# Kernel optimization log

Measured on AMD Instinct MI355X. Metric: run time of the kernel, lower is better.

## Reference

```python
import jax, jax.numpy as jnp
import numpy as np

EP = 1e-4
MAX_ITER = 100
L = [512, 512]          # context lengths
C = 256                 # padded feature dim == total_dim
HEADS = 2


def nonsat_activation(x, ep=EP, max_iter=MAX_ITER):
    # Fixed-point iteration y <- (2y^3/3 + x)/(y^2+1), y0 = x.
    # Matches torch version: iterate on detached values, final update uses live x.
    xd = jax.lax.stop_gradient(x)
    f = lambda y: (2.0 * y ** 3 / 3.0 + xd) / (y ** 2 + 1.0)

    def cond(s):
        y, y_new, i = s
        return jnp.logical_and(jnp.mean(jnp.abs(y_new - y)) > ep, i <= max_iter)

    def body(s):
        y, y_new, i = s
        return (y_new, f(y_new), i + 1)

    y_prev, _, _ = jax.lax.while_loop(cond, body, (xd, f(xd), 0))
    y_prev = jax.lax.stop_gradient(y_prev)
    # final (returned) update, differentiable w.r.t. x only
    return (2.0 * y_prev ** 3 / 3.0 + x) / (y_prev ** 2 + 1.0)


def setup_inputs() -> dict:
    key = jax.random.key(0)
    k1, k2, k3 = jax.random.split(key, 3)
    x1 = jax.random.normal(k1, (32, 512, 256), dtype=jnp.float32)
    x2 = jax.random.normal(k2, (32, 512, 192), dtype=jnp.float32)
    # xavier_normal_ for U: std = sqrt(2/(fan_in+fan_out)) = sqrt(2/512) = 1/16
    U = jax.random.normal(k3, (HEADS, C, C), dtype=jnp.float32) * (1.0 / 16.0)
    return {"x1": x1, "x2": x2, "U": U}


def reference(x1, x2, U):
    # pad contexts to common feature dim C (zeros on the right)
    contexts = [x1, jnp.pad(x2, ((0, 0), (0, 0), (0, C - x2.shape[-1])))]
    q = sum(L)
    scaling = C ** (-0.5)
    M = jnp.concatenate(contexts, axis=1)  # (B, q, C)

    # mask uses sizes = L[1:] with blocks starting at offset 0 (faithful quirk)
    mask_mul = jnp.ones((q, q), dtype=jnp.float32).at[:L[1], :L[1]].set(0.0)

    h_reps = []
    mask_add = None
    for h in range(HEADS):
        # K[b,i,j] = sum_{c,d} M[b,i,c] U[h,c,d] M[b,j,d]
        K = jnp.einsum('bic,cd,bjd->bij', M, U[h], M) * scaling
        K = nonsat_activation(K)
        if mask_add is None:  # cached after head 0, reused for later heads
            mask_add = jnp.zeros((q, q), dtype=jnp.float32).at[:L[1], :L[1]].set(jnp.min(K))
        K_hat = K * mask_mul + mask_add
        cols = jnp.max(K_hat, axis=1)   # (B, q) max over rows per column
        rows = jnp.max(K_hat, axis=2)   # (B, q) max over cols per row
        alpha = rows + cols             # (B, q)
        reps = []
        offset = 0
        for i, Ci in enumerate(contexts):
            a = alpha[:, offset:offset + L[i]]          # (B, l_i)
            offset += L[i]
            wt = jax.nn.softmax(a, axis=1)              # (B, l_i)
            r = jnp.einsum('bl,blc->bc', wt, Ci)        # (B, C)
            reps.append(r)
        h_reps.append(jnp.stack(reps, axis=1))          # (B, N, C)
    return jnp.stack(h_reps, axis=0)                    # (heads, B, N, C)
```

## Files before the change

kernel.cpp:

```cpp
#include <hip/hip_runtime.h>
#include <math.h>

typedef _Float16 h16;
typedef h16  h16x8 __attribute__((ext_vector_type(8)));
typedef h16  h16x4 __attribute__((ext_vector_type(4)));
typedef float f32x4 __attribute__((ext_vector_type(4)));

#define MH_OFF   ((size_t)0)
#define ML_OFF   (MH_OFF + 16777216)
#define UHT_OFF  (ML_OFF + 16777216)
#define ULT_OFF  (UHT_OFF + 262144)
#define RMA_OFF  (ULT_OFF + 262144)
#define RMH_OFF  (RMA_OFF + 262144)
#define PCM_OFF  (RMH_OFF + 262144)
#define M0_OFF   (PCM_OFF + 4194304)

__device__ __forceinline__ float nonsat(float x) {
    float y = x;
#pragma unroll
    for (int i = 0; i < 24; ++i) {
        float y2 = y * y;
        y = fmaf(0.66666667f * y, y2, x) / (y2 + 1.0f);
    }
    return y;
}

__device__ __forceinline__ int fkey(float f) {
    const int i = __float_as_int(f);
    return (i >= 0) ? i : (i ^ 0x7fffffff);
}
__device__ __forceinline__ float funkey(int k) {
    return __int_as_float((k >= 0) ? k : (k ^ 0x7fffffff));
}

__global__ void k_prep(const float* __restrict__ x1, const float* __restrict__ x2,
                       const float* __restrict__ U, h16* __restrict__ MH,
                       h16* __restrict__ ML, h16* __restrict__ UHt,
                       h16* __restrict__ ULt, int* __restrict__ m0key) {
    const int gid = blockIdx.x * 256 + threadIdx.x;
    if (blockIdx.x < 8192) {
        const int g  = gid;
        const int d4 = (g & 63) * 4;
        const int j  = (g >> 6) & 1023;
        const int b  = g >> 16;
        float v[4];
        if (j < 512) {
            const float* p = x1 + ((size_t)(b * 512 + j) * 256 + d4);
#pragma unroll
            for (int k = 0; k < 4; ++k) v[k] = p[k];
        } else {
            const float* p = x2 + (size_t)(b * 512 + (j - 512)) * 192;
#pragma unroll
            for (int k = 0; k < 4; ++k) {
                const int c = d4 + k;
                v[k] = (c < 192) ? p[c] : 0.0f;
            }
        }
        h16x4 hh, ll;
#pragma unroll
        for (int k = 0; k < 4; ++k) {
            const h16 hi = (h16)v[k];
            hh[k] = hi;
            ll[k] = (h16)(v[k] - (float)hi);
        }
        const size_t o = (size_t)g * 4;
        *(h16x4*)&MH[o] = hh;
        *(h16x4*)&ML[o] = ll;
    } else {
        const int g = gid - 8192 * 256;
        if (g < 32768) {
            const int c4 = (g & 63) * 4;
            const int d  = (g >> 6) & 255;
            const int h  = g >> 14;
            h16x4 hh, ll;
#pragma unroll
            for (int k = 0; k < 4; ++k) {
                const float v = U[((size_t)h * 256 + c4 + k) * 256 + d] * 4.0f;
                const h16 hi = (h16)v;
                hh[k] = hi;
                ll[k] = (h16)(v - (float)hi);
            }
            const size_t o = ((size_t)h * 256 + d) * 256 + c4;
            *(h16x4*)&UHt[o] = hh;
            *(h16x4*)&ULt[o] = ll;
        } else if (g == 32768) {
            *m0key = 0x7fffffff;
        }
    }
}

__global__ __launch_bounds__(256, 2)
void k_main(const h16* __restrict__ MH, const h16* __restrict__ ML,
            const h16* __restrict__ UHt, const h16* __restrict__ ULt,
            float* __restrict__ rmax_all, float* __restrict__ rmax_hi,
            float* __restrict__ pcm, int* __restrict__ m0key) {
    __shared__ __align__(16) h16 sP[2][64 * 256];
    __shared__ float red[512 + 4];

    const int n    = blockIdx.x;
    const int x    = n & 7;
    const int s    = n >> 3;
    const int b    = x + 8 * (s >> 5);
    const int h    = (s >> 4) & 1;
    const int rblk = s & 15;
    const int hb   = h * 32 + b;
    const int r0   = rblk * 64;
    const int t    = threadIdx.x;
    const int w    = t >> 6;
    const int l    = t & 63;
    const int q    = l >> 4;
    const int ln   = l & 15;

    {
        f32x4 acc[4][4];
        const f32x4 z4 = {0.f, 0.f, 0.f, 0.f};
#pragma unroll
        for (int i = 0; i < 4; ++i)
#pragma unroll
            for (int j = 0; j < 4; ++j) acc[i][j] = z4;

        for (int kc = 0; kc < 8; ++kc) {
            const int c0 = kc * 32;
            h16x8 aH[4], aL[4], bH[4], bL[4];
#pragma unroll
            for (int ti = 0; ti < 4; ++ti) {
                const size_t off =
                    (size_t)(b * 1024 + r0 + ti * 16 + ln) * 256 + c0 + q * 8;
                aH[ti] = *(const h16x8*)&MH[off];
                aL[ti] = *(const h16x8*)&ML[off];
            }
#pragma unroll
            for (int tj = 0; tj < 4; ++tj) {
                const size_t off =
                    (size_t)(h * 256 + w * 64 + tj * 16 + ln) * 256 + c0 + q * 8;
                bH[tj] = *(const h16x8*)&UHt[off];
                bL[tj] = *(const h16x8*)&ULt[off];
            }
#pragma unroll
            for (int ti = 0; ti < 4; ++ti)
#pragma unroll
                for (int tj = 0; tj < 4; ++tj)
                    acc[ti][tj] = __builtin_amdgcn_mfma_f32_16x16x32_f16(
                        aH[ti], bH[tj], acc[ti][tj], 0, 0, 0);
#pragma unroll
            for (int ti = 0; ti < 4; ++ti)
#pragma unroll
                for (int tj = 0; tj < 4; ++tj)
                    acc[ti][tj] = __builtin_amdgcn_mfma_f32_16x16x32_f16(
                        aL[ti], bH[tj], acc[ti][tj], 0, 0, 0);
#pragma unroll
            for (int ti = 0; ti < 4; ++ti)
#pragma unroll
                for (int tj = 0; tj < 4; ++tj)
                    acc[ti][tj] = __builtin_amdgcn_mfma_f32_16x16x32_f16(
                        aH[ti], bL[tj], acc[ti][tj], 0, 0, 0);
        }
#pragma unroll
        for (int ti = 0; ti < 4; ++ti)
#pragma unroll
            for (int tj = 0; tj < 4; ++tj)
#pragma unroll
                for (int reg = 0; reg < 4; ++reg) {
                    const int r = ti * 16 + q * 4 + reg;
                    const int d = w * 64 + tj * 16 + ln;
                    const float v = acc[ti][tj][reg];
                    const h16 hi = (h16)v;
                    const h16 lo = (h16)(v - (float)hi);
                    const int off = r * 256 + (((d >> 3) ^ (r & 7)) << 3) + (d & 7);
                    sP[0][off] = hi;
                    sP[1][off] = lo;
                }
    }
    __syncthreads();

    float gmin = INFINITY;

    for (int jt = 0; jt < 2; ++jt) {
        const int jbase = jt * 512 + w * 128;
        f32x4 acc[4][8];
        const f32x4 z4 = {0.f, 0.f, 0.f, 0.f};
#pragma unroll
        for (int i = 0; i < 4; ++i)
#pragma unroll
            for (int j = 0; j < 8; ++j) acc[i][j] = z4;

        for (int kc = 0; kc < 8; ++kc) {
            const int d0 = kc * 32;
            h16x8 aH[4], aL[4], bb[8];
#pragma unroll
            for (int ti = 0; ti < 4; ++ti) {
                const int r = ti * 16 + ln;
                const int g = (kc * 4 + q) ^ (r & 7);
                aH[ti] = *(const h16x8*)&sP[0][r * 256 + g * 8];
                aL[ti] = *(const h16x8*)&sP[1][r * 256 + g * 8];
            }
#pragma unroll
            for (int tj = 0; tj < 8; ++tj)
                bb[tj] = *(const h16x8*)&MH[
                    (size_t)(b * 1024 + jbase + tj * 16 + ln) * 256 + d0 + q * 8];
#pragma unroll
            for (int tj = 0; tj < 8; ++tj)
#pragma unroll
                for (int ti = 0; ti < 4; ++ti)
                    acc[ti][tj] = __builtin_amdgcn_mfma_f32_16x16x32_f16(
                        aH[ti], bb[tj], acc[ti][tj], 0, 0, 0);
#pragma unroll
            for (int tj = 0; tj < 8; ++tj)
#pragma unroll
                for (int ti = 0; ti < 4; ++ti)
                    acc[ti][tj] = __builtin_amdgcn_mfma_f32_16x16x32_f16(
                        aL[ti], bb[tj], acc[ti][tj], 0, 0, 0);
#pragma unroll
            for (int tj = 0; tj < 8; ++tj)
                bb[tj] = *(const h16x8*)&ML[
                    (size_t)(b * 1024 + jbase + tj * 16 + ln) * 256 + d0 + q * 8];
#pragma unroll
            for (int tj = 0; tj < 8; ++tj)
#pragma unroll
                for (int ti = 0; ti < 4; ++ti)
                    acc[ti][tj] = __builtin_amdgcn_mfma_f32_16x16x32_f16(
                        aH[ti], bb[tj], acc[ti][tj], 0, 0, 0);
        }

#pragma unroll
        for (int ti = 0; ti < 4; ++ti)
#pragma unroll
            for (int reg = 0; reg < 4; ++reg) {
                float m = acc[ti][0][reg];
#pragma unroll
                for (int tj = 1; tj < 8; ++tj) m = fmaxf(m, acc[ti][tj][reg]);
                m = fmaxf(m, __shfl_xor(m, 1));
                m = fmaxf(m, __shfl_xor(m, 2));
                m = fmaxf(m, __shfl_xor(m, 4));
                m = fmaxf(m, __shfl_xor(m, 8));
                if (ln == 0)
                    red[(jt * 4 + w) * 64 + ti * 16 + q * 4 + reg] = m;
            }
#pragma unroll
        for (int tj = 0; tj < 8; ++tj) {
            float m = -INFINITY;
#pragma unroll
            for (int ti = 0; ti < 4; ++ti)
#pragma unroll
                for (int reg = 0; reg < 4; ++reg) m = fmaxf(m, acc[ti][tj][reg]);
            m = fmaxf(m, __shfl_xor(m, 16));
            m = fmaxf(m, __shfl_xor(m, 32));
            if (q == 0)
                pcm[(size_t)(hb * 16 + rblk) * 1024 + jbase + tj * 16 + ln] =
                    m * 0.015625f;
        }
#pragma unroll
        for (int ti = 0; ti < 4; ++ti)
#pragma unroll
            for (int tj = 0; tj < 8; ++tj)
#pragma unroll
                for (int reg = 0; reg < 4; ++reg)
                    gmin = fminf(gmin, acc[ti][tj][reg]);
    }

#pragma unroll
    for (int off = 1; off < 64; off <<= 1) gmin = fminf(gmin, __shfl_xor(gmin, off));
    if (l == 0) red[512 + w] = gmin;
    __syncthreads();

    if (t < 64) {
        float a = -INFINITY, hh = -INFINITY;
#pragma unroll
        for (int w2 = 0; w2 < 4; ++w2) {
            a  = fmaxf(a,  red[w2 * 64 + t]);
            const float v1 = red[(4 + w2) * 64 + t];
            a  = fmaxf(a, v1);
            hh = fmaxf(hh, v1);
        }
        rmax_all[(size_t)hb * 1024 + r0 + t] = a  * 0.015625f;
        rmax_hi [(size_t)hb * 1024 + r0 + t] = hh * 0.015625f;
    }
    if (t == 0 && hb < 32) {
        const float g4 = fminf(fminf(red[512], red[513]),
                               fminf(red[514], red[515])) * 0.015625f;
        atomicMin(m0key, fkey(g4));
    }
}

__global__ __launch_bounds__(256)
void k_fin(const float* __restrict__ rmax_all, const float* __restrict__ rmax_hi,
           const float* __restrict__ pcm, const int* __restrict__ m0key,
           const float* __restrict__ x1, const float* __restrict__ x2,
           float* __restrict__ out) {
    __shared__ float wv[512];
    __shared__ float sm[4], ss[4];
    const int blk = blockIdx.x;
    const int seg = blk & 1;
    const int hb  = blk >> 1;
    const int b   = hb & 31;
    const int t   = threadIdx.x;
    const float m0 = funkey(*m0key);

    float a2[2];
#pragma unroll
    for (int half = 0; half < 2; ++half) {
        const int i = seg * 512 + half * 256 + t;
        float rraw;
        if (seg == 0) rraw = fmaxf(m0, rmax_hi[(size_t)hb * 1024 + i]);
        else          rraw = rmax_all[(size_t)hb * 1024 + i];
        float call = -INFINITY, chi = -INFINITY;
#pragma unroll
        for (int rb = 0; rb < 16; ++rb) {
            const float v = pcm[(size_t)(hb * 16 + rb) * 1024 + i];
            call = fmaxf(call, v);
            if (rb >= 8) chi = fmaxf(chi, v);
        }
        const float craw = (seg == 0) ? fmaxf(m0, chi) : call;
        a2[half] = nonsat(rraw) + nonsat(craw);
    }
    const float a0 = a2[0], a1 = a2[1];

    float m = fmaxf(a0, a1);
#pragma unroll
    for (int off = 1; off < 64; off <<= 1) m = fmaxf(m, __shfl_xor(m, off));
    if ((t & 63) == 0) sm[t >> 6] = m;
    __syncthreads();
    const float amax = fmaxf(fmaxf(sm[0], sm[1]), fmaxf(sm[2], sm[3]));

    const float e0 = __expf(a0 - amax), e1 = __expf(a1 - amax);
    wv[t] = e0; wv[t + 256] = e1;
    float s = e0 + e1;
#pragma unroll
    for (int off = 1; off < 64; off <<= 1) s += __shfl_xor(s, off);
    if ((t & 63) == 0) ss[t >> 6] = s;
    __syncthreads();
    const float inv = 1.0f / (ss[0] + ss[1] + ss[2] + ss[3]);

    float acc = 0.0f;
    if (seg == 0) {
        const float* xp = x1 + (size_t)b * 512 * 256 + t;
#pragma unroll 4
        for (int l = 0; l < 512; ++l) acc = fmaf(wv[l], xp[(size_t)l * 256], acc);
        out[blk * 256 + t] = acc * inv;
    } else {
        if (t < 192) {
            const float* xp = x2 + (size_t)b * 512 * 192 + t;
#pragma unroll 4
            for (int l = 0; l < 512; ++l) acc = fmaf(wv[l], xp[(size_t)l * 192], acc);
            out[blk * 256 + t] = acc * inv;
        } else {
            out[blk * 256 + t] = 0.0f;
        }
    }
}

extern "C" void kernel_launch(void* const* d_in, const int* in_sizes, int n_in,
                              void* d_out, int out_size, void* d_ws, size_t ws_size,
                              hipStream_t stream) {
    const float* x1 = (const float*)d_in[0];
    const float* x2 = (const float*)d_in[1];
    const float* U  = (const float*)d_in[2];
    float* out = (float*)d_out;
    char* wsb  = (char*)d_ws;

    h16*   MHp  = (h16*)(wsb + MH_OFF);
    h16*   MLp  = (h16*)(wsb + ML_OFF);
    h16*   UHt  = (h16*)(wsb + UHT_OFF);
    h16*   ULt  = (h16*)(wsb + ULT_OFF);
    float* rma  = (float*)(wsb + RMA_OFF);
    float* rmh  = (float*)(wsb + RMH_OFF);
    float* pcm  = (float*)(wsb + PCM_OFF);
    int*   m0k  = (int*)(wsb + M0_OFF);

    hipLaunchKernelGGL(k_prep, dim3(8321), dim3(256), 0, stream, x1, x2, U,
                       MHp, MLp, UHt, ULt, m0k);
    hipLaunchKernelGGL(k_main, dim3(1024), dim3(256), 0, stream, MHp, MLp,
                       UHt, ULt, rma, rmh, pcm, m0k);
    hipLaunchKernelGGL(k_fin,  dim3(128),  dim3(256), 0, stream, rma, rmh,
                       pcm, m0k, x1, x2, out);
}
```

Before: 296.9 us.

## Halve k_main row tile to 32 rows, doubling blocks and occupancy

Shrinks each k_main block from 64 to 32 query rows and splits the column sweep into four 256-wide chunks, cutting accumulator registers and shared memory so four blocks can fit per CU instead of two. Row maxima are now carried in registers across chunks and reduced once at the end, rather than written to shared memory per chunk. The grid doubles to 2048 blocks and the per-column partial-max buffer doubles, so k_fin now reduces 32 partials per column. The cost is more re-reading of M and U per output and a smaller MFMA tile per wave, which lowers operand reuse.

```diff
diff --git a/kernel.cpp b/kernel.cpp
--- a/kernel.cpp
+++ b/kernel.cpp
@@ -13,7 +13,7 @@
 #define RMA_OFF  (ULT_OFF + 262144)
 #define RMH_OFF  (RMA_OFF + 262144)
 #define PCM_OFF  (RMH_OFF + 262144)
-#define M0_OFF   (PCM_OFF + 4194304)
+#define M0_OFF   (PCM_OFF + 8388608)
 
 __device__ __forceinline__ float nonsat(float x) {
     float y = x;
@@ -89,22 +89,22 @@
     }
 }
 
-__global__ __launch_bounds__(256, 2)
+__global__ __launch_bounds__(256, 4)
 void k_main(const h16* __restrict__ MH, const h16* __restrict__ ML,
             const h16* __restrict__ UHt, const h16* __restrict__ ULt,
             float* __restrict__ rmax_all, float* __restrict__ rmax_hi,
             float* __restrict__ pcm, int* __restrict__ m0key) {
-    __shared__ __align__(16) h16 sP[2][64 * 256];
-    __shared__ float red[512 + 4];
+    __shared__ __align__(16) h16 sP[2][32 * 256];
+    __shared__ float red[256 + 4];
 
     const int n    = blockIdx.x;
     const int x    = n & 7;
     const int s    = n >> 3;
-    const int b    = x + 8 * (s >> 5);
-    const int h    = (s >> 4) & 1;
-    const int rblk = s & 15;
+    const int b    = x + 8 * (s >> 6);
+    const int h    = (s >> 5) & 1;
+    const int rb   = s & 31;
     const int hb   = h * 32 + b;
-    const int r0   = rblk * 64;
+    const int r0   = rb * 32;
     const int t    = threadIdx.x;
     const int w    = t >> 6;
     const int l    = t & 63;
@@ -112,18 +112,18 @@
     const int ln   = l & 15;
 
     {
-        f32x4 acc[4][4];
+        f32x4 acc[2][4];
         const f32x4 z4 = {0.f, 0.f, 0.f, 0.f};
 #pragma unroll
-        for (int i = 0; i < 4; ++i)
+        for (int i = 0; i < 2; ++i)
 #pragma unroll
             for (int j = 0; j < 4; ++j) acc[i][j] = z4;
 
         for (int kc = 0; kc < 8; ++kc) {
             const int c0 = kc * 32;
-            h16x8 aH[4], aL[4], bH[4], bL[4];
-#pragma unroll
-            for (int ti = 0; ti < 4; ++ti) {
+            h16x8 aH[2], aL[2], bH[4], bL[4];
+#pragma unroll
+            for (int ti = 0; ti < 2; ++ti) {
                 const size_t off =
                     (size_t)(b * 1024 + r0 + ti * 16 + ln) * 256 + c0 + q * 8;
                 aH[ti] = *(const h16x8*)&MH[off];
@@ -137,26 +137,26 @@
                 bL[tj] = *(const h16x8*)&ULt[off];
             }
 #pragma unroll
-            for (int ti = 0; ti < 4; ++ti)
+            for (int ti = 0; ti < 2; ++ti)
 #pragma unroll
                 for (int tj = 0; tj < 4; ++tj)
                     acc[ti][tj] = __builtin_amdgcn_mfma_f32_16x16x32_f16(
                         aH[ti], bH[tj], acc[ti][tj], 0, 0, 0);
 #pragma unroll
-            for (int ti = 0; ti < 4; ++ti)
+            for (int ti = 0; ti < 2; ++ti)
 #pragma unroll
                 for (int tj = 0; tj < 4; ++tj)
                     acc[ti][tj] = __builtin_amdgcn_mfma_f32_16x16x32_f16(
                         aL[ti], bH[tj], acc[ti][tj], 0, 0, 0);
 #pragma unroll
-            for (int ti = 0; ti < 4; ++ti)
+            for (int ti = 0; ti < 2; ++ti)
 #pragma unroll
                 for (int tj = 0; tj < 4; ++tj)
                     acc[ti][tj] = __builtin_amdgcn_mfma_f32_16x16x32_f16(
                         aH[ti], bL[tj], acc[ti][tj], 0, 0, 0);
         }
 #pragma unroll
-        for (int ti = 0; ti < 4; ++ti)
+        for (int ti = 0; ti < 2; ++ti)
 #pragma unroll
             for (int tj = 0; tj < 4; ++tj)
 #pragma unroll
@@ -173,111 +173,128 @@
     }
     __syncthreads();
 
+    float rA[8], rH[8];
+#pragma unroll
+    for (int i = 0; i < 8; ++i) { rA[i] = -INFINITY; rH[i] = -INFINITY; }
     float gmin = INFINITY;
 
-    for (int jt = 0; jt < 2; ++jt) {
-        const int jbase = jt * 512 + w * 128;
-        f32x4 acc[4][8];
+    for (int jt = 0; jt < 4; ++jt) {
+        const int jbase = jt * 256 + w * 64;
+        f32x4 acc[2][4];
         const f32x4 z4 = {0.f, 0.f, 0.f, 0.f};
 #pragma unroll
-        for (int i = 0; i < 4; ++i)
-#pragma unroll
-            for (int j = 0; j < 8; ++j) acc[i][j] = z4;
+        for (int i = 0; i < 2; ++i)
+#pragma unroll
+            for (int j = 0; j < 4; ++j) acc[i][j] = z4;
 
         for (int kc = 0; kc < 8; ++kc) {
             const int d0 = kc * 32;
-            h16x8 aH[4], aL[4], bb[8];
-#pragma unroll
-            for (int ti = 0; ti < 4; ++ti) {
+            h16x8 aH[2], aL[2], bb[4];
+#pragma unroll
+            for (int ti = 0; ti < 2; ++ti) {
                 const int r = ti * 16 + ln;
                 const int g = (kc * 4 + q) ^ (r & 7);
                 aH[ti] = *(const h16x8*)&sP[0][r * 256 + g * 8];
                 aL[ti] = *(const h16x8*)&sP[1][r * 256 + g * 8];
             }
 #pragma unroll
-            for (int tj = 0; tj < 8; ++tj)
+            for (int tj = 0; tj < 4; ++tj)
                 bb[tj] = *(const h16x8*)&MH[
                     (size_t)(b * 1024 + jbase + tj * 16 + ln) * 256 + d0 + q * 8];
 #pragma unroll
-            for (int tj = 0; tj < 8; ++tj)
-#pragma unroll
-                for (int ti = 0; ti < 4; ++ti)
+            for (int tj = 0; tj < 4; ++tj)
+#pragma unroll
+                for (int ti = 0; ti < 2; ++ti)
                     acc[ti][tj] = __builtin_amdgcn_mfma_f32_16x16x32_f16(
                         aH[ti], bb[tj], acc[ti][tj], 0, 0, 0);
 #pragma unroll
-            for (int tj = 0; tj < 8; ++tj)
-#pragma unroll
-                for (int ti = 0; ti < 4; ++ti)
+            for (int tj = 0; tj < 4; ++tj)
+#pragma unroll
+                for (int ti = 0; ti < 2; ++ti)
                     acc[ti][tj] = __builtin_amdgcn_mfma_f32_16x16x32_f16(
                         aL[ti], bb[tj], acc[ti][tj], 0, 0, 0);
 #pragma unroll
-            for (int tj = 0; tj < 8; ++tj)
+            for (int tj = 0; tj < 4; ++tj)
                 bb[tj] = *(const h16x8*)&ML[
                     (size_t)(b * 1024 + jbase + tj * 16 + ln) * 256 + d0 + q * 8];
 #pragma unroll
-            for (int tj = 0; tj < 8; ++tj)
-#pragma unroll
-                for (int ti = 0; ti < 4; ++ti)
+            for (int tj = 0; tj < 4; ++tj)
+#pragma unroll
+                for (int ti = 0; ti < 2; ++ti)
                     acc[ti][tj] = __builtin_amdgcn_mfma_f32_16x16x32_f16(
                         aH[ti], bb[tj], acc[ti][tj], 0, 0, 0);
         }
 
-#pragma unroll
-        for (int ti = 0; ti < 4; ++ti)
+        const bool hij = (jt >= 2);
+#pragma unroll
+        for (int ti = 0; ti < 2; ++ti)
 #pragma unroll
             for (int reg = 0; reg < 4; ++reg) {
                 float m = acc[ti][0][reg];
-#pragma unroll
-                for (int tj = 1; tj < 8; ++tj) m = fmaxf(m, acc[ti][tj][reg]);
-                m = fmaxf(m, __shfl_xor(m, 1));
-                m = fmaxf(m, __shfl_xor(m, 2));
-                m = fmaxf(m, __shfl_xor(m, 4));
-                m = fmaxf(m, __shfl_xor(m, 8));
-                if (ln == 0)
-                    red[(jt * 4 + w) * 64 + ti * 16 + q * 4 + reg] = m;
-            }
-#pragma unroll
-        for (int tj = 0; tj < 8; ++tj) {
+                m = fmaxf(m, acc[ti][1][reg]);
+                m = fmaxf(m, acc[ti][2][reg]);
+                m = fmaxf(m, acc[ti][3][reg]);
+                const int idx = ti * 4 + reg;
+                rA[idx] = fmaxf(rA[idx], m);
+                if (hij) rH[idx] = fmaxf(rH[idx], m);
+            }
+#pragma unroll
+        for (int tj = 0; tj < 4; ++tj) {
             float m = -INFINITY;
 #pragma unroll
-            for (int ti = 0; ti < 4; ++ti)
+            for (int ti = 0; ti < 2; ++ti)
 #pragma unroll
                 for (int reg = 0; reg < 4; ++reg) m = fmaxf(m, acc[ti][tj][reg]);
             m = fmaxf(m, __shfl_xor(m, 16));
             m = fmaxf(m, __shfl_xor(m, 32));
             if (q == 0)
-                pcm[(size_t)(hb * 16 + rblk) * 1024 + jbase + tj * 16 + ln] =
+                pcm[(size_t)(hb * 32 + rb) * 1024 + jbase + tj * 16 + ln] =
                     m * 0.015625f;
         }
 #pragma unroll
-        for (int ti = 0; ti < 4; ++ti)
-#pragma unroll
-            for (int tj = 0; tj < 8; ++tj)
+        for (int ti = 0; ti < 2; ++ti)
+#pragma unroll
+            for (int tj = 0; tj < 4; ++tj)
 #pragma unroll
                 for (int reg = 0; reg < 4; ++reg)
                     gmin = fminf(gmin, acc[ti][tj][reg]);
     }
 
 #pragma unroll
+    for (int ti = 0; ti < 2; ++ti)
+#pragma unroll
+        for (int reg = 0; reg < 4; ++reg) {
+            const int idx = ti * 4 + reg;
+            float a = rA[idx], hh = rH[idx];
+#pragma unroll
+            for (int o2 = 1; o2 < 16; o2 <<= 1) {
+                a  = fmaxf(a,  __shfl_xor(a,  o2));
+                hh = fmaxf(hh, __shfl_xor(hh, o2));
+            }
+            if (ln == 0) {
+                const int row = ti * 16 + q * 4 + reg;
+                red[w * 32 + row]       = a;
+                red[128 + w * 32 + row] = hh;
+            }
+        }
+#pragma unroll
     for (int off = 1; off < 64; off <<= 1) gmin = fminf(gmin, __shfl_xor(gmin, off));
-    if (l == 0) red[512 + w] = gmin;
+    if (l == 0) red[256 + w] = gmin;
     __syncthreads();
 
-    if (t < 64) {
+    if (t < 32) {
         float a = -INFINITY, hh = -INFINITY;
 #pragma unroll
         for (int w2 = 0; w2 < 4; ++w2) {
-            a  = fmaxf(a,  red[w2 * 64 + t]);
-            const float v1 = red[(4 + w2) * 64 + t];
-            a  = fmaxf(a, v1);
-            hh = fmaxf(hh, v1);
+            a  = fmaxf(a,  red[w2 * 32 + t]);
+            hh = fmaxf(hh, red[128 + w2 * 32 + t]);
         }
         rmax_all[(size_t)hb * 1024 + r0 + t] = a  * 0.015625f;
         rmax_hi [(size_t)hb * 1024 + r0 + t] = hh * 0.015625f;
     }
     if (t == 0 && hb < 32) {
-        const float g4 = fminf(fminf(red[512], red[513]),
-                               fminf(red[514], red[515])) * 0.015625f;
+        const float g4 = fminf(fminf(red[256], red[257]),
+                               fminf(red[258], red[259])) * 0.015625f;
         atomicMin(m0key, fkey(g4));
     }
 }
@@ -305,10 +322,10 @@
         else          rraw = rmax_all[(size_t)hb * 1024 + i];
         float call = -INFINITY, chi = -INFINITY;
 #pragma unroll
-        for (int rb = 0; rb < 16; ++rb) {
-            const float v = pcm[(size_t)(hb * 16 + rb) * 1024 + i];
+        for (int rb = 0; rb < 32; ++rb) {
+            const float v = pcm[(size_t)(hb * 32 + rb) * 1024 + i];
             call = fmaxf(call, v);
-            if (rb >= 8) chi = fmaxf(chi, v);
+            if (rb >= 16) chi = fmaxf(chi, v);
         }
         const float craw = (seg == 0) ? fmaxf(m0, chi) : call;
         a2[half] = nonsat(rraw) + nonsat(craw);
@@ -369,7 +386,7 @@
 
     hipLaunchKernelGGL(k_prep, dim3(8321), dim3(256), 0, stream, x1, x2, U,
                        MHp, MLp, UHt, ULt, m0k);
-    hipLaunchKernelGGL(k_main, dim3(1024), dim3(256), 0, stream, MHp, MLp,
+    hipLaunchKernelGGL(k_main, dim3(2048), dim3(256), 0, stream, MHp, MLp,
                        UHt, ULt, rma, rmh, pcm, m0k);
     hipLaunchKernelGGL(k_fin,  dim3(128),  dim3(256), 0, stream, rma, rmh,
                        pcm, m0k, x1, x2, out);
```

Measured after the change: 536.9 us. 80.8% more time.

## Shrink second GEMM tile to 4x4 per wave and accumulate row maxima in registers

Applied to the files above, without the earlier changes.

The second-stage GEMM now uses four column passes of 64 columns per wave instead of two passes of 128, halving the accumulator array so register pressure drops and occupancy may rise. Row maxima are kept in per-thread registers across passes and reduced with shuffles once at the end, replacing per-pass LDS writes. Both hi and lo B fragments are loaded up front, the k-loops are partially unrolled, and x1 is read with a vectorized float4 load in the prep kernel. The trade-off is that each A fragment from LDS is reused across fewer columns, so LDS traffic and loop overhead per MFMA increase.

```diff
diff --git a/kernel.cpp b/kernel.cpp
--- a/kernel.cpp
+++ b/kernel.cpp
@@ -45,9 +45,8 @@
         const int b  = g >> 16;
         float v[4];
         if (j < 512) {
-            const float* p = x1 + ((size_t)(b * 512 + j) * 256 + d4);
-#pragma unroll
-            for (int k = 0; k < 4; ++k) v[k] = p[k];
+            const float4 p = *(const float4*)(x1 + ((size_t)(b * 512 + j) * 256 + d4));
+            v[0] = p.x; v[1] = p.y; v[2] = p.z; v[3] = p.w;
         } else {
             const float* p = x2 + (size_t)(b * 512 + (j - 512)) * 192;
 #pragma unroll
@@ -119,6 +118,7 @@
 #pragma unroll
             for (int j = 0; j < 4; ++j) acc[i][j] = z4;
 
+#pragma unroll 2
         for (int kc = 0; kc < 8; ++kc) {
             const int c0 = kc * 32;
             h16x8 aH[4], aL[4], bH[4], bL[4];
@@ -173,20 +173,31 @@
     }
     __syncthreads();
 
+    float rA[16], rH[16];
+#pragma unroll
+    for (int i = 0; i < 16; ++i) { rA[i] = -INFINITY; rH[i] = -INFINITY; }
     float gmin = INFINITY;
 
-    for (int jt = 0; jt < 2; ++jt) {
-        const int jbase = jt * 512 + w * 128;
-        f32x4 acc[4][8];
+    for (int jt = 0; jt < 4; ++jt) {
+        const int jbase = jt * 256 + w * 64;
+        f32x4 acc[4][4];
         const f32x4 z4 = {0.f, 0.f, 0.f, 0.f};
 #pragma unroll
         for (int i = 0; i < 4; ++i)
 #pragma unroll
-            for (int j = 0; j < 8; ++j) acc[i][j] = z4;
-
+            for (int j = 0; j < 4; ++j) acc[i][j] = z4;
+
+#pragma unroll 2
         for (int kc = 0; kc < 8; ++kc) {
             const int d0 = kc * 32;
-            h16x8 aH[4], aL[4], bb[8];
+            h16x8 bbH[4], bbL[4], aH[4], aL[4];
+#pragma unroll
+            for (int tj = 0; tj < 4; ++tj) {
+                const size_t off =
+                    (size_t)(b * 1024 + jbase + tj * 16 + ln) * 256 + d0 + q * 8;
+                bbH[tj] = *(const h16x8*)&MH[off];
+                bbL[tj] = *(const h16x8*)&ML[off];
+            }
 #pragma unroll
             for (int ti = 0; ti < 4; ++ti) {
                 const int r = ti * 16 + ln;
@@ -195,49 +206,40 @@
                 aL[ti] = *(const h16x8*)&sP[1][r * 256 + g * 8];
             }
 #pragma unroll
-            for (int tj = 0; tj < 8; ++tj)
-                bb[tj] = *(const h16x8*)&MH[
-                    (size_t)(b * 1024 + jbase + tj * 16 + ln) * 256 + d0 + q * 8];
-#pragma unroll
-            for (int tj = 0; tj < 8; ++tj)
+            for (int tj = 0; tj < 4; ++tj)
 #pragma unroll
                 for (int ti = 0; ti < 4; ++ti)
                     acc[ti][tj] = __builtin_amdgcn_mfma_f32_16x16x32_f16(
-                        aH[ti], bb[tj], acc[ti][tj], 0, 0, 0);
-#pragma unroll
-            for (int tj = 0; tj < 8; ++tj)
+                        aH[ti], bbH[tj], acc[ti][tj], 0, 0, 0);
+#pragma unroll
+            for (int tj = 0; tj < 4; ++tj)
 #pragma unroll
                 for (int ti = 0; ti < 4; ++ti)
                     acc[ti][tj] = __builtin_amdgcn_mfma_f32_16x16x32_f16(
-                        aL[ti], bb[tj], acc[ti][tj], 0, 0, 0);
-#pragma unroll
-            for (int tj = 0; tj < 8; ++tj)
-                bb[tj] = *(const h16x8*)&ML[
-                    (size_t)(b * 1024 + jbase + tj * 16 + ln) * 256 + d0 + q * 8];
-#pragma unroll
-            for (int tj = 0; tj < 8; ++tj)
+                        aL[ti], bbH[tj], acc[ti][tj], 0, 0, 0);
+#pragma unroll
+            for (int tj = 0; tj < 4; ++tj)
 #pragma unroll
                 for (int ti = 0; ti < 4; ++ti)
                     acc[ti][tj] = __builtin_amdgcn_mfma_f32_16x16x32_f16(
-                        aH[ti], bb[tj], acc[ti][tj], 0, 0, 0);
-        }
-
+                        aH[ti], bbL[tj], acc[ti][tj], 0, 0, 0);
+        }
+
+        const bool hij = (jt >= 2);
 #pragma unroll
         for (int ti = 0; ti < 4; ++ti)
 #pragma unroll
             for (int reg = 0; reg < 4; ++reg) {
                 float m = acc[ti][0][reg];
-#pragma unroll
-                for (int tj = 1; tj < 8; ++tj) m = fmaxf(m, acc[ti][tj][reg]);
-                m = fmaxf(m, __shfl_xor(m, 1));
-                m = fmaxf(m, __shfl_xor(m, 2));
-                m = fmaxf(m, __shfl_xor(m, 4));
-                m = fmaxf(m, __shfl_xor(m, 8));
-                if (ln == 0)
-                    red[(jt * 4 + w) * 64 + ti * 16 + q * 4 + reg] = m;
-            }
-#pragma unroll
-        for (int tj = 0; tj < 8; ++tj) {
+                m = fmaxf(m, acc[ti][1][reg]);
+                m = fmaxf(m, acc[ti][2][reg]);
+                m = fmaxf(m, acc[ti][3][reg]);
+                const int idx = ti * 4 + reg;
+                rA[idx] = fmaxf(rA[idx], m);
+                if (hij) rH[idx] = fmaxf(rH[idx], m);
+            }
+#pragma unroll
+        for (int tj = 0; tj < 4; ++tj) {
             float m = -INFINITY;
 #pragma unroll
             for (int ti = 0; ti < 4; ++ti)
@@ -252,12 +254,29 @@
 #pragma unroll
         for (int ti = 0; ti < 4; ++ti)
 #pragma unroll
-            for (int tj = 0; tj < 8; ++tj)
+            for (int tj = 0; tj < 4; ++tj)
 #pragma unroll
                 for (int reg = 0; reg < 4; ++reg)
                     gmin = fminf(gmin, acc[ti][tj][reg]);
     }
 
+#pragma unroll
+    for (int ti = 0; ti < 4; ++ti)
+#pragma unroll
+        for (int reg = 0; reg < 4; ++reg) {
+            const int idx = ti * 4 + reg;
+            float a = rA[idx], hh = rH[idx];
+#pragma unroll
+            for (int o2 = 1; o2 < 16; o2 <<= 1) {
+                a  = fmaxf(a,  __shfl_xor(a,  o2));
+                hh = fmaxf(hh, __shfl_xor(hh, o2));
+            }
+            if (ln == 0) {
+                const int row = ti * 16 + q * 4 + reg;
+                red[w * 64 + row]       = a;
+                red[256 + w * 64 + row] = hh;
+            }
+        }
 #pragma unroll
     for (int off = 1; off < 64; off <<= 1) gmin = fminf(gmin, __shfl_xor(gmin, off));
     if (l == 0) red[512 + w] = gmin;
@@ -268,9 +287,7 @@
 #pragma unroll
         for (int w2 = 0; w2 < 4; ++w2) {
             a  = fmaxf(a,  red[w2 * 64 + t]);
-            const float v1 = red[(4 + w2) * 64 + t];
-            a  = fmaxf(a, v1);
-            hh = fmaxf(hh, v1);
+            hh = fmaxf(hh, red[256 + w2 * 64 + t]);
         }
         rmax_all[(size_t)hb * 1024 + r0 + t] = a  * 0.015625f;
         rmax_hi [(size_t)hb * 1024 + r0 + t] = hh * 0.015625f;
```

Result: slower. 305.2 us (+2.8%).

## Split final reduction across chunks with atomics, stagger k-loop order, vectorize prep loads

Applied to the files above, without the earlier changes.

The final weighted-sum kernel now splits each sequence into two 256-row chunks, doubling the block count, and accumulates results with atomicAdd into an output that the prep kernel zeroes beforehand. The main kernel rotates its k-chunk and j-tile iteration order per wave and block so that concurrent waves touch different memory regions, which is meant to reduce bank and channel contention. The prep kernel also uses float4 loads for the inputs. The atomics make the floating-point summation order nondeterministic, and the extra zeroing blocks add a little work to prep.

```diff
diff --git a/kernel.cpp b/kernel.cpp
--- a/kernel.cpp
+++ b/kernel.cpp
@@ -36,7 +36,8 @@
 __global__ void k_prep(const float* __restrict__ x1, const float* __restrict__ x2,
                        const float* __restrict__ U, h16* __restrict__ MH,
                        h16* __restrict__ ML, h16* __restrict__ UHt,
-                       h16* __restrict__ ULt, int* __restrict__ m0key) {
+                       h16* __restrict__ ULt, int* __restrict__ m0key,
+                       float* __restrict__ out) {
     const int gid = blockIdx.x * 256 + threadIdx.x;
     if (blockIdx.x < 8192) {
         const int g  = gid;
@@ -45,16 +46,14 @@
         const int b  = g >> 16;
         float v[4];
         if (j < 512) {
-            const float* p = x1 + ((size_t)(b * 512 + j) * 256 + d4);
-#pragma unroll
-            for (int k = 0; k < 4; ++k) v[k] = p[k];
+            const float4 p = *(const float4*)(x1 + ((size_t)(b * 512 + j) * 256 + d4));
+            v[0] = p.x; v[1] = p.y; v[2] = p.z; v[3] = p.w;
+        } else if (d4 < 192) {
+            const float4 p = *(const float4*)(x2 +
+                (size_t)(b * 512 + (j - 512)) * 192 + d4);
+            v[0] = p.x; v[1] = p.y; v[2] = p.z; v[3] = p.w;
         } else {
-            const float* p = x2 + (size_t)(b * 512 + (j - 512)) * 192;
-#pragma unroll
-            for (int k = 0; k < 4; ++k) {
-                const int c = d4 + k;
-                v[k] = (c < 192) ? p[c] : 0.0f;
-            }
+            v[0] = v[1] = v[2] = v[3] = 0.0f;
         }
         h16x4 hh, ll;
 #pragma unroll
@@ -66,26 +65,26 @@
         const size_t o = (size_t)g * 4;
         *(h16x4*)&MH[o] = hh;
         *(h16x4*)&ML[o] = ll;
+    } else if (blockIdx.x < 8320) {
+        const int g  = gid - 8192 * 256;
+        const int c4 = (g & 63) * 4;
+        const int d  = (g >> 6) & 255;
+        const int h  = g >> 14;
+        h16x4 hh, ll;
+#pragma unroll
+        for (int k = 0; k < 4; ++k) {
+            const float v = U[((size_t)h * 256 + c4 + k) * 256 + d] * 4.0f;
+            const h16 hi = (h16)v;
+            hh[k] = hi;
+            ll[k] = (h16)(v - (float)hi);
+        }
+        const size_t o = ((size_t)h * 256 + d) * 256 + c4;
+        *(h16x4*)&UHt[o] = hh;
+        *(h16x4*)&ULt[o] = ll;
     } else {
-        const int g = gid - 8192 * 256;
-        if (g < 32768) {
-            const int c4 = (g & 63) * 4;
-            const int d  = (g >> 6) & 255;
-            const int h  = g >> 14;
-            h16x4 hh, ll;
-#pragma unroll
-            for (int k = 0; k < 4; ++k) {
-                const float v = U[((size_t)h * 256 + c4 + k) * 256 + d] * 4.0f;
-                const h16 hi = (h16)v;
-                hh[k] = hi;
-                ll[k] = (h16)(v - (float)hi);
-            }
-            const size_t o = ((size_t)h * 256 + d) * 256 + c4;
-            *(h16x4*)&UHt[o] = hh;
-            *(h16x4*)&ULt[o] = ll;
-        } else if (g == 32768) {
-            *m0key = 0x7fffffff;
-        }
+        const int z = gid - 8320 * 256;
+        out[z] = 0.0f;
+        if (z == 0) *m0key = 0x7fffffff;
     }
 }
 
@@ -110,6 +109,7 @@
     const int l    = t & 63;
     const int q    = l >> 4;
     const int ln   = l & 15;
+    const int phase = (w + s) & 3;
 
     {
         f32x4 acc[4][4];
@@ -119,7 +119,8 @@
 #pragma unroll
             for (int j = 0; j < 4; ++j) acc[i][j] = z4;
 
-        for (int kc = 0; kc < 8; ++kc) {
+        for (int kcl = 0; kcl < 8; ++kcl) {
+            const int kc = (kcl + phase * 2) & 7;
             const int c0 = kc * 32;
             h16x8 aH[4], aL[4], bH[4], bL[4];
 #pragma unroll
@@ -175,7 +176,8 @@
 
     float gmin = INFINITY;
 
-    for (int jt = 0; jt < 2; ++jt) {
+    for (int jtl = 0; jtl < 2; ++jtl) {
+        const int jt = (jtl + (phase & 1)) & 1;
         const int jbase = jt * 512 + w * 128;
         f32x4 acc[4][8];
         const f32x4 z4 = {0.f, 0.f, 0.f, 0.f};
@@ -184,7 +186,8 @@
 #pragma unroll
             for (int j = 0; j < 8; ++j) acc[i][j] = z4;
 
-        for (int kc = 0; kc < 8; ++kc) {
+        for (int kcl = 0; kcl < 8; ++kcl) {
+            const int kc = (kcl + phase * 2) & 7;
             const int d0 = kc * 32;
             h16x8 aH[4], aL[4], bb[8];
 #pragma unroll
@@ -289,12 +292,13 @@
            float* __restrict__ out) {
     __shared__ float wv[512];
     __shared__ float sm[4], ss[4];
-    const int blk = blockIdx.x;
-    const int seg = blk & 1;
-    const int hb  = blk >> 1;
-    const int b   = hb & 31;
-    const int t   = threadIdx.x;
-    const float m0 = funkey(*m0key);
+    const int blk   = blockIdx.x;
+    const int chunk = blk & 1;
+    const int seg   = (blk >> 1) & 1;
+    const int hb    = blk >> 2;
+    const int b     = hb & 31;
+    const int t     = threadIdx.x;
+    const float m0  = funkey(*m0key);
 
     float a2[2];
 #pragma unroll
@@ -331,21 +335,20 @@
     __syncthreads();
     const float inv = 1.0f / (ss[0] + ss[1] + ss[2] + ss[3]);
 
+    const int lo = chunk * 256;
     float acc = 0.0f;
     if (seg == 0) {
-        const float* xp = x1 + (size_t)b * 512 * 256 + t;
+        const float* xp = x1 + ((size_t)b * 512 + lo) * 256 + t;
 #pragma unroll 4
-        for (int l = 0; l < 512; ++l) acc = fmaf(wv[l], xp[(size_t)l * 256], acc);
-        out[blk * 256 + t] = acc * inv;
-    } else {
-        if (t < 192) {
-            const float* xp = x2 + (size_t)b * 512 * 192 + t;
+        for (int l = 0; l < 256; ++l)
+            acc = fmaf(wv[lo + l], xp[(size_t)l * 256], acc);
+        atomicAdd(&out[(hb * 2 + seg) * 256 + t], acc * inv);
+    } else if (t < 192) {
+        const float* xp = x2 + ((size_t)b * 512 + lo) * 192 + t;
 #pragma unroll 4
-            for (int l = 0; l < 512; ++l) acc = fmaf(wv[l], xp[(size_t)l * 192], acc);
-            out[blk * 256 + t] = acc * inv;
-        } else {
-            out[blk * 256 + t] = 0.0f;
-        }
+        for (int l = 0; l < 256; ++l)
+            acc = fmaf(wv[lo + l], xp[(size_t)l * 192], acc);
+        atomicAdd(&out[(hb * 2 + seg) * 256 + t], acc * inv);
     }
 }
 
@@ -367,10 +370,10 @@
     float* pcm  = (float*)(wsb + PCM_OFF);
     int*   m0k  = (int*)(wsb + M0_OFF);
 
-    hipLaunchKernelGGL(k_prep, dim3(8321), dim3(256), 0, stream, x1, x2, U,
-                       MHp, MLp, UHt, ULt, m0k);
+    hipLaunchKernelGGL(k_prep, dim3(8448), dim3(256), 0, stream, x1, x2, U,
+                       MHp, MLp, UHt, ULt, m0k, out);
     hipLaunchKernelGGL(k_main, dim3(1024), dim3(256), 0, stream, MHp, MLp,
                        UHt, ULt, rma, rmh, pcm, m0k);
-    hipLaunchKernelGGL(k_fin,  dim3(128),  dim3(256), 0, stream, rma, rmh,
+    hipLaunchKernelGGL(k_fin,  dim3(256),  dim3(256), 0, stream, rma, rmh,
                        pcm, m0k, x1, x2, out);
 }
```

Result: faster. 287.1 us (-3.3%).
